# Optimization experiments

Measured on AMD Instinct MI355X. Metric: run time of the kernel, lower is better.

Reference implementation:

```python
import jax, jax.numpy as jnp
import numpy as np

B, TQ, TKV, D, H = 4, 512, 4096, 1024, 8
HEAD_DIM = D // H


def setup_inputs() -> dict:
    key = jax.random.key(0)
    ks = jax.random.split(key, 8)
    s = 0.02
    inputs_q = jax.random.normal(ks[0], (B, TQ, D), jnp.float32)
    inputs_kv = jax.random.normal(ks[1], (B, TKV, D), jnp.float32)
    attention_mask = jax.random.randint(ks[2], (B, TQ, TKV), 0, 2).astype(bool)
    Wq = jax.random.normal(ks[3], (D, D), jnp.float32) * s
    Wk = jax.random.normal(ks[4], (D, D), jnp.float32) * s
    Wv = jax.random.normal(ks[5], (D, D), jnp.float32) * s
    Wo = jax.random.normal(ks[6], (D, D), jnp.float32) * s
    zb = jnp.zeros((D,), jnp.float32)
    return {"inputs_q": inputs_q, "inputs_kv": inputs_kv, "attention_mask": attention_mask,
            "Wq": Wq, "bq": zb, "Wk": Wk, "bk": zb, "Wv": Wv, "bv": zb, "Wo": Wo, "bo": zb}


def _split_heads(x, h):
    b, t, c = x.shape
    return x.reshape(b, t, h, c // h).transpose(0, 2, 1, 3)  # b h t d


def reference(inputs_q, inputs_kv, attention_mask, Wq, bq, Wk, bk, Wv, bv, Wo, bo):
    q = _split_heads(inputs_q @ Wq + bq, H)   # [b,h,tq,d]
    k = _split_heads(inputs_kv @ Wk + bk, H)  # [b,h,tkv,d]
    v = _split_heads(inputs_kv @ Wv + bv, H)  # [b,h,tkv,d]
    scale = 1.0 / np.sqrt(HEAD_DIM).astype(np.float32)
    scores = jnp.einsum('bhtd,bhTd->bhtT', q, k) * scale
    large_k = jnp.asarray(1e30, scores.dtype)  # 1e30 for fp32 per source
    scores = jnp.where(attention_mask[:, None, :, :], scores, -large_k)
    probs = jax.nn.softmax(scores, axis=-1)
    summed = jnp.einsum('bhtT,bhTd->bhtd', probs, v)
    b, h, t, d = summed.shape
    summed = summed.transpose(0, 2, 1, 3).reshape(b, t, h * d)  # [b,tq,hiddens]
    # wipe rows whose mask is entirely zero (post-softmax wipe-masking)
    wipe = jnp.all(~attention_mask, axis=-1, keepdims=True)  # [b,tq,1]
    summed = jnp.where(wipe, jnp.zeros_like(summed), summed)
    return summed @ Wo + bo
```

## Files before the change

kernel.cpp:

```cpp
#include <hip/hip_runtime.h>
#include <cstdint>
#include <cstddef>

typedef unsigned short US;
typedef __bf16 bf16_t;
typedef bf16_t bf16x8 __attribute__((ext_vector_type(8)));
typedef float  f32x4  __attribute__((ext_vector_type(4)));
typedef US     us8    __attribute__((ext_vector_type(8)));
typedef US     us4    __attribute__((ext_vector_type(4)));

#define AS1 __attribute__((address_space(1)))
#define AS3 __attribute__((address_space(3)))

__device__ __forceinline__ void gl_lds16(const void* g, void* l) {
    __builtin_amdgcn_global_load_lds((AS1 unsigned int*)(size_t)g,
                                     (AS3 unsigned int*)l, 16, 0, 0);
}

__device__ __forceinline__ US f2bf(float f) {
    unsigned u = __builtin_bit_cast(unsigned, f);
    u += 0x7FFFu + ((u >> 16) & 1u);
    return (US)(u >> 16);
}

__device__ __forceinline__ float bf2f(US u) {
    return __builtin_bit_cast(float, (unsigned)u << 16);
}

__device__ __forceinline__ bf16x8 ldv8(const US* p) {
    return __builtin_bit_cast(bf16x8, *(const us8*)p);
}

__global__ void prep(const float* __restrict__ Xq, const float* __restrict__ Xkv,
                     const int* __restrict__ Mi, unsigned long long* __restrict__ MBits,
                     US* __restrict__ XqB, US* __restrict__ XkvB,
                     const float* __restrict__ Wq, const float* __restrict__ Wk,
                     const float* __restrict__ Wv, const float* __restrict__ Wo,
                     US* __restrict__ WTbase) {
    __shared__ float t[32][33];
    const int b = blockIdx.x, tid = threadIdx.x;

    for (int u = b; u < 18432; u += 4096) {
        if (u < 2048) {
            int i = u * 256 + tid;
            float4 f = ((const float4*)Xq)[i];
            us4 o = { f2bf(f.x), f2bf(f.y), f2bf(f.z), f2bf(f.w) };
            ((us4*)XqB)[i] = o;
        } else {
            int i = (u - 2048) * 256 + tid;
            float4 f = ((const float4*)Xkv)[i];
            us4 o = { f2bf(f.x), f2bf(f.y), f2bf(f.z), f2bf(f.w) };
            ((us4*)XkvB)[i] = o;
        }
    }

    for (int u = b; u < 32768; u += 4096) {
        int i = u * 256 + tid;
        int m = Mi[i];
        unsigned long long bits = __ballot(m != 0);
        if ((tid & 63) == 0) MBits[i >> 6] = bits;
    }

    {
        int z = b >> 10, rr = b & 1023;
        int bx = rr & 31, by = rr >> 5;
        const float* W = (z == 0) ? Wq : (z == 1) ? Wk : (z == 2) ? Wv : Wo;
        US* WT = WTbase + (size_t)z * 1024 * 1024;
        int tx = tid & 31, ty = tid >> 5;
        int x = bx * 32 + tx;
#pragma unroll
        for (int r = 0; r < 4; ++r)
            t[ty + r * 8][tx] = W[(size_t)(by * 32 + ty + r * 8) * 1024 + x];
        __syncthreads();
        int nx = by * 32 + tx;
#pragma unroll
        for (int r = 0; r < 4; ++r)
            WT[(size_t)(bx * 32 + ty + r * 8) * 1024 + nx] = f2bf(t[tx][ty + r * 8]);
    }
}

template <int MODE, int BM>
__global__ __launch_bounds__(256, 2)
void gemm_bt(const US* __restrict__ A, const US* __restrict__ Bt,
             const float* __restrict__ bias, void* __restrict__ out,
             int tlog2, float scale) {
    constexpr int K = 1024, N = 1024, BK = 64;
    constexpr int MI = BM / 32;
    __shared__ US As[BM * BK];
    __shared__ US Bs[128 * BK];
    const int tid = threadIdx.x;
    const int wv = tid >> 6, ln = tid & 63;
    const int g = ln >> 4, c15 = ln & 15;
    const int m0 = blockIdx.x * BM, n0 = blockIdx.y * 128;
    const int wm = (wv & 1) * (BM / 2), wn = (wv >> 1) * 64;

    f32x4 acc[MI][4];
    const f32x4 z = {0.f, 0.f, 0.f, 0.f};
#pragma unroll
    for (int i = 0; i < MI; ++i)
#pragma unroll
        for (int j = 0; j < 4; ++j) acc[i][j] = z;

    const US* Ab = A + (size_t)m0 * K;
    const US* Bb = Bt + (size_t)n0 * K;

    for (int k0 = 0; k0 < K; k0 += BK) {
        __syncthreads();
#pragma unroll
        for (int q = 0; q < BM / 32; ++q) {
            int eb = (q * 256 + wv * 64) * 8;
            int r = (eb >> 6) + (ln >> 3);
            int sw = (ln & 7) ^ (r & 7);
            gl_lds16(Ab + (size_t)r * K + k0 + sw * 8, &As[eb]);
        }
#pragma unroll
        for (int q = 0; q < 4; ++q) {
            int eb = (q * 256 + wv * 64) * 8;
            int r = (eb >> 6) + (ln >> 3);
            int sw = (ln & 7) ^ (r & 7);
            gl_lds16(Bb + (size_t)r * K + k0 + sw * 8, &Bs[eb]);
        }
        __syncthreads();
#pragma unroll
        for (int ks = 0; ks < 2; ++ks) {
            bf16x8 a[MI], b[4];
#pragma unroll
            for (int i = 0; i < MI; ++i) {
                int p = (ks * 4 + g) ^ (c15 & 7);
                a[i] = ldv8(&As[(wm + i * 16 + c15) * BK + p * 8]);
            }
#pragma unroll
            for (int j = 0; j < 4; ++j) {
                int p = (ks * 4 + g) ^ (c15 & 7);
                b[j] = ldv8(&Bs[(wn + j * 16 + c15) * BK + p * 8]);
            }
#pragma unroll
            for (int i = 0; i < MI; ++i)
#pragma unroll
                for (int j = 0; j < 4; ++j)
                    acc[i][j] = __builtin_amdgcn_mfma_f32_16x16x32_bf16(a[i], b[j], acc[i][j], 0, 0, 0);
        }
    }

#pragma unroll
    for (int i = 0; i < MI; ++i) {
#pragma unroll
        for (int j = 0; j < 4; ++j) {
            int col = n0 + wn + j * 16 + c15;
            float bvv = bias[col];
#pragma unroll
            for (int r = 0; r < 4; ++r) {
                int row = m0 + wm + i * 16 + g * 4 + r;
                float v = (acc[i][j][r] + bvv) * scale;
                if (MODE == 0) {
                    int b_ = row >> tlog2;
                    int t = row & ((1 << tlog2) - 1);
                    int h = col >> 7, d = col & 127;
                    ((US*)out)[(((size_t)(b_ * 8 + h) << tlog2) + t) * 128 + d] = f2bf(v);
                } else {
                    ((float*)out)[(size_t)row * N + col] = v;
                }
            }
        }
    }
}

__global__ __launch_bounds__(256, 2)
void gemm_kv(const US* __restrict__ A, const US* __restrict__ BtK,
             const US* __restrict__ BtV, const float* __restrict__ bk,
             const float* __restrict__ bv, US* __restrict__ Kout,
             US* __restrict__ VTout) {
    constexpr int K = 1024, BK = 64;
    __shared__ US lds[3 * 128 * BK];
    US* As  = lds;
    US* BsK = lds + 128 * BK;
    US* BsV = lds + 2 * 128 * BK;
    const int tid = threadIdx.x;
    const int wv = tid >> 6, ln = tid & 63;
    const int g = ln >> 4, c15 = ln & 15;
    const int m0 = blockIdx.x * 128, n0 = blockIdx.y * 128;
    const int wm = (wv & 1) * 64, wn = (wv >> 1) * 64;

    f32x4 aK[4][4], aV[4][4];
    const f32x4 z = {0.f, 0.f, 0.f, 0.f};
#pragma unroll
    for (int i = 0; i < 4; ++i)
#pragma unroll
        for (int j = 0; j < 4; ++j) { aK[i][j] = z; aV[i][j] = z; }

    const US* Ab  = A   + (size_t)m0 * K;
    const US* BbK = BtK + (size_t)n0 * K;
    const US* BbV = BtV + (size_t)n0 * K;

    for (int k0 = 0; k0 < K; k0 += BK) {
        __syncthreads();
#pragma unroll
        for (int q = 0; q < 4; ++q) {
            int eb = (q * 256 + wv * 64) * 8;
            int r = (eb >> 6) + (ln >> 3);
            int sw = (ln & 7) ^ (r & 7);
            gl_lds16(Ab  + (size_t)r * K + k0 + sw * 8, &As[eb]);
            gl_lds16(BbK + (size_t)r * K + k0 + sw * 8, &BsK[eb]);
            gl_lds16(BbV + (size_t)r * K + k0 + sw * 8, &BsV[eb]);
        }
        __syncthreads();
#pragma unroll
        for (int ks = 0; ks < 2; ++ks) {
            bf16x8 a[4], bK[4], bV[4];
#pragma unroll
            for (int i = 0; i < 4; ++i) {
                int p = (ks * 4 + g) ^ (c15 & 7);
                a[i] = ldv8(&As[(wm + i * 16 + c15) * BK + p * 8]);
            }
#pragma unroll
            for (int j = 0; j < 4; ++j) {
                int p = (ks * 4 + g) ^ (c15 & 7);
                bK[j] = ldv8(&BsK[(wn + j * 16 + c15) * BK + p * 8]);
                bV[j] = ldv8(&BsV[(wn + j * 16 + c15) * BK + p * 8]);
            }
#pragma unroll
            for (int i = 0; i < 4; ++i)
#pragma unroll
                for (int j = 0; j < 4; ++j) {
                    aK[i][j] = __builtin_amdgcn_mfma_f32_16x16x32_bf16(a[i], bK[j], aK[i][j], 0, 0, 0);
                    aV[i][j] = __builtin_amdgcn_mfma_f32_16x16x32_bf16(a[i], bV[j], aV[i][j], 0, 0, 0);
                }
        }
    }

    const int h = n0 >> 7;
    const int b_ = m0 >> 12, tbase = m0 & 4095;

#pragma unroll
    for (int i = 0; i < 4; ++i) {
#pragma unroll
        for (int j = 0; j < 4; ++j) {
            int col = n0 + wn + j * 16 + c15;
            float bkv = bk[col];
            int d = col & 127;
#pragma unroll
            for (int r = 0; r < 4; ++r) {
                int row = m0 + wm + i * 16 + g * 4 + r;
                int t = row & 4095;
                Kout[(((size_t)(b_ * 8 + h) << 12) + t) * 128 + d] = f2bf(aK[i][j][r] + bkv);
            }
        }
    }

    __syncthreads();
    US* T = lds;
#pragma unroll
    for (int i = 0; i < 4; ++i) {
#pragma unroll
        for (int j = 0; j < 4; ++j) {
            int dcol = wn + j * 16 + c15;
            float bvv = bv[n0 + dcol];
#pragma unroll
            for (int r = 0; r < 4; ++r) {
                int kvrow = wm + i * 16 + g * 4 + r;
                T[dcol * 136 + kvrow] = f2bf(aV[i][j][r] + bvv);
            }
        }
    }
    __syncthreads();
    {
        int d = tid >> 1, half = (tid & 1) * 64;
        US* vrow = VTout + ((size_t)(b_ * 8 + h) * 128 + d) * 4096 + tbase + half;
        const US* tr = &T[d * 136 + half];
#pragma unroll
        for (int s = 0; s < 8; ++s)
            *(us8*)(vrow + s * 8) = *(const us8*)(tr + s * 8);
    }
}

__global__ __launch_bounds__(256, 3)
void flash(const US* __restrict__ Qh, const US* __restrict__ Kh,
           const US* __restrict__ VTh, const unsigned long long* __restrict__ MBits,
           US* __restrict__ Opart, float* __restrict__ Lpart) {
    __shared__ US Ks[64 * 128];
    __shared__ US Vs[128 * 64];
    __shared__ US Ps[4][32 * 64];
    const int tid = threadIdx.x, wv = tid >> 6, ln = tid & 63;
    const int g = ln >> 4, c15 = ln & 15;
    const int bid = blockIdx.x;
    const int qt = bid / 192;
    const int rest = bid - qt * 192;
    const int bh = rest / 6, sp = rest - bh * 6;
    const int qbase = qt * 128;
    const int b_ = bh >> 3;
    const int t0 = (sp < 4) ? sp * 11 : 44 + (sp - 4) * 10;
    const int nt = (sp < 4) ? 11 : 10;
    const int wq = wv * 32;

    bf16x8 qa[2][4];
#pragma unroll
    for (int ib = 0; ib < 2; ++ib) {
        const US* qrow = Qh + ((size_t)bh * 512 + qbase + wq + ib * 16 + c15) * 128;
#pragma unroll
        for (int ks = 0; ks < 4; ++ks)
            qa[ib][ks] = ldv8(qrow + ks * 32 + g * 8);
    }

    f32x4 o[8][2];
    const f32x4 z = {0.f, 0.f, 0.f, 0.f};
#pragma unroll
    for (int d = 0; d < 8; ++d) { o[d][0] = z; o[d][1] = z; }
    float l2[2] = {0.f, 0.f};

    const unsigned long long* Mrow[2];
    Mrow[0] = MBits + (size_t)(b_ * 512 + qbase + wq + c15) * 64;
    Mrow[1] = Mrow[0] + (size_t)16 * 64;
    const US* Kbase = Kh + ((size_t)bh * 4096 + (size_t)t0 * 64) * 128;
    const US* Vbase = VTh + (size_t)bh * 128 * 4096;
    US* Pw = &Ps[wv][0];

    for (int t = 0; t < nt; ++t) {
        int kv0 = (t0 + t) * 64;
        __syncthreads();
        const US* Kb = Kbase + (size_t)t * 64 * 128;
#pragma unroll
        for (int q = 0; q < 4; ++q) {
            int eb = (q * 256 + wv * 64) * 8;
            int r = (eb >> 7) + (ln >> 4);
            int sw = (ln & 15) ^ (r & 15);
            gl_lds16(Kb + (size_t)r * 128 + sw * 8, &Ks[eb]);
        }
#pragma unroll
        for (int q = 0; q < 4; ++q) {
            int eb = (q * 256 + wv * 64) * 8;
            int r = (eb >> 6) + (ln >> 3);
            int sw = (ln & 7) ^ (r & 7);
            gl_lds16(Vbase + (size_t)r * 4096 + kv0 + sw * 8, &Vs[eb]);
        }
        unsigned long long m64[2];
        m64[0] = Mrow[0][t0 + t];
        m64[1] = Mrow[1][t0 + t];
        __syncthreads();

#pragma unroll
        for (int kb = 0; kb < 4; ++kb) {
            f32x4 s0 = z, s1 = z;
#pragma unroll
            for (int ks = 0; ks < 4; ++ks) {
                bf16x8 kf = ldv8(&Ks[(kb * 16 + c15) * 128 + (((ks * 4 + g) ^ c15) * 8)]);
                s0 = __builtin_amdgcn_mfma_f32_16x16x32_bf16(kf, qa[0][ks], s0, 0, 0, 0);
                s1 = __builtin_amdgcn_mfma_f32_16x16x32_bf16(kf, qa[1][ks], s1, 0, 0, 0);
            }
            int cw = kb * 4 + g;
#pragma unroll
            for (int ib = 0; ib < 2; ++ib) {
                f32x4 sv = ib ? s1 : s0;
                unsigned mq = (unsigned)(m64[ib] >> (kb * 16 + g * 4)) & 15u;
                float p0 = (mq & 1u) ? __expf(sv[0]) : 0.f;
                float p1 = (mq & 2u) ? __expf(sv[1]) : 0.f;
                float p2 = (mq & 4u) ? __expf(sv[2]) : 0.f;
                float p3 = (mq & 8u) ? __expf(sv[3]) : 0.f;
                l2[ib] += (p0 + p1) + (p2 + p3);
                int q = ib * 16 + c15;
                US* wp = Pw + q * 64 + (((cw >> 1) ^ (q & 7)) * 8) + (cw & 1) * 4;
                us4 pv = { f2bf(p0), f2bf(p1), f2bf(p2), f2bf(p3) };
                *(us4*)wp = pv;
            }
        }

#pragma unroll
        for (int ks = 0; ks < 2; ++ks) {
            bf16x8 pf[2];
#pragma unroll
            for (int ib = 0; ib < 2; ++ib) {
                int q = ib * 16 + c15;
                pf[ib] = ldv8(&Pw[q * 64 + (((ks * 4 + g) ^ (q & 7)) * 8)]);
            }
#pragma unroll
            for (int d = 0; d < 8; ++d) {
                bf16x8 vf = ldv8(&Vs[(d * 16 + c15) * 64 + (((ks * 4 + g) ^ (c15 & 7)) * 8)]);
                o[d][0] = __builtin_amdgcn_mfma_f32_16x16x32_bf16(vf, pf[0], o[d][0], 0, 0, 0);
                o[d][1] = __builtin_amdgcn_mfma_f32_16x16x32_bf16(vf, pf[1], o[d][1], 0, 0, 0);
            }
        }
    }

    float lf[2];
#pragma unroll
    for (int ib = 0; ib < 2; ++ib) {
        float l = l2[ib];
        l += __shfl_xor(l, 16); l += __shfl_xor(l, 32);
        lf[ib] = l;
    }
    if (ln < 16) {
        size_t lb = ((size_t)sp * 32 + bh) * 512 + qbase + wq + c15;
        Lpart[lb] = lf[0];
        Lpart[lb + 16] = lf[1];
    }
    US* Ob = Opart + (((size_t)sp * 32 + bh) * 128 + g * 4) * 512 + qbase + wq + c15;
#pragma unroll
    for (int d = 0; d < 8; ++d)
#pragma unroll
        for (int r = 0; r < 4; ++r) {
            Ob[(size_t)(d * 16 + r) * 512] = f2bf(o[d][0][r]);
            Ob[(size_t)(d * 16 + r) * 512 + 16] = f2bf(o[d][1][r]);
        }
}

__global__ void combine(const US* __restrict__ Opart, const float* __restrict__ Lpart,
                        US* __restrict__ AO) {
    __shared__ float linv[128];
    __shared__ float T[128 * 33];
    const int qt = blockIdx.x, bh = blockIdx.y;
    const int b_ = bh >> 3, h = bh & 7;
    const int tid = threadIdx.x;
    const size_t spstride = (size_t)32 * 128 * 512;

    if (tid < 128) {
        float s = 0.f;
#pragma unroll
        for (int sp = 0; sp < 6; ++sp)
            s += Lpart[((size_t)sp * 32 + bh) * 512 + qt * 128 + tid];
        linv[tid] = (s > 0.f) ? 1.f / s : 0.f;
    }
    __syncthreads();

    for (int ds0 = 0; ds0 < 128; ds0 += 32) {
        if (ds0) __syncthreads();
        {
            int d = ds0 + (tid >> 3);
            int q0 = (tid & 7) * 16;
            const US* base = Opart + ((size_t)bh * 128 + d) * 512 + qt * 128 + q0;
            float acc[16];
#pragma unroll
            for (int i = 0; i < 16; ++i) acc[i] = 0.f;
#pragma unroll
            for (int sp = 0; sp < 6; ++sp) {
                us8 a = *(const us8*)(base + sp * spstride);
                us8 b = *(const us8*)(base + sp * spstride + 8);
#pragma unroll
                for (int i = 0; i < 8; ++i) {
                    acc[i] += bf2f(a[i]);
                    acc[8 + i] += bf2f(b[i]);
                }
            }
            int dd = d - ds0;
#pragma unroll
            for (int i = 0; i < 16; ++i)
                T[(q0 + i) * 33 + dd] = acc[i] * linv[q0 + i];
        }
        __syncthreads();
#pragma unroll
        for (int it = 0; it < 4; ++it) {
            int idx = tid + it * 256;
            int q = idx >> 3, c = idx & 7;
            const float* tr = &T[q * 33 + c * 4];
            us4 ov = { f2bf(tr[0]), f2bf(tr[1]), f2bf(tr[2]), f2bf(tr[3]) };
            *(us4*)(AO + ((size_t)(b_ * 512 + qt * 128 + q)) * 1024 + h * 128 + ds0 + c * 4) = ov;
        }
    }
}

extern "C" void kernel_launch(void* const* d_in, const int* in_sizes, int n_in,
                              void* d_out, int out_size, void* d_ws, size_t ws_size,
                              hipStream_t stream) {
    (void)in_sizes; (void)n_in; (void)out_size; (void)ws_size;
    const float* Xq  = (const float*)d_in[0];
    const float* Xkv = (const float*)d_in[1];
    const int*   Mi  = (const int*)d_in[2];
    const float* Wq  = (const float*)d_in[3];
    const float* bq  = (const float*)d_in[4];
    const float* Wk  = (const float*)d_in[5];
    const float* bk  = (const float*)d_in[6];
    const float* Wv  = (const float*)d_in[7];
    const float* bv  = (const float*)d_in[8];
    const float* Wo  = (const float*)d_in[9];
    const float* bo  = (const float*)d_in[10];
    float* out = (float*)d_out;

    char* p = (char*)d_ws;
    US* WT   = (US*)p; p += (size_t)4 * 1024 * 1024 * 2;
    US* AO   = (US*)p; p += (size_t)2048 * 1024 * 2;
    US* XqB  = (US*)p; p += (size_t)2048 * 1024 * 2;
    US* Qh   = (US*)p; p += (size_t)2048 * 1024 * 2;
    US* Kh   = (US*)p; p += (size_t)16384 * 1024 * 2;
    US* VTh  = (US*)p; p += (size_t)16384 * 1024 * 2;
    US* XkvB = (US*)p; p += (size_t)16384 * 1024 * 2;
    unsigned long long* MBits = (unsigned long long*)p; p += (size_t)131072 * 8;
    US* Opart    = XkvB;
    float* Lpart = (float*)XqB;

    prep<<<4096, 256, 0, stream>>>(Xq, Xkv, Mi, MBits, XqB, XkvB, Wq, Wk, Wv, Wo, WT);

    gemm_bt<0, 64><<<dim3(32, 8), 256, 0, stream>>>(XqB, WT, bq, Qh, 9, 0.08838834764831843f);
    gemm_kv<<<dim3(128, 8), 256, 0, stream>>>(XkvB, WT + 1048576, WT + 2097152,
                                              bk, bv, Kh, VTh);
    flash<<<768, 256, 0, stream>>>(Qh, Kh, VTh, MBits, Opart, Lpart);
    combine<<<dim3(4, 32), 256, 0, stream>>>(Opart, Lpart, AO);
    gemm_bt<1, 64><<<dim3(32, 8), 256, 0, stream>>>(AO, WT + 3145728, bo, out, 0, 1.0f);
}
```

Before: 340.5 us.

## Double flash query tile per block and split KV into eight chunks

Each flash block now processes 256 query rows, 64 per wave, instead of 128, so every K/V tile staged in LDS is reused across twice as many queries. The KV sequence is split into 8 equal chunks of 8 tiles, replacing the uneven 6-way split, and the grid shrinks from 768 to 512 blocks. The combine kernel now sums 8 partials. The cost is roughly double the accumulator and Q-fragment registers, a doubled P buffer in LDS, and occupancy lowered from 3 to 2 blocks per CU, which reduces latency hiding.

```diff
diff --git a/kernel.cpp b/kernel.cpp
--- a/kernel.cpp
+++ b/kernel.cpp
@@ -273,48 +273,50 @@
     }
 }
 
-__global__ __launch_bounds__(256, 3)
+__global__ __launch_bounds__(256, 2)
 void flash(const US* __restrict__ Qh, const US* __restrict__ Kh,
            const US* __restrict__ VTh, const unsigned long long* __restrict__ MBits,
            US* __restrict__ Opart, float* __restrict__ Lpart) {
     __shared__ US Ks[64 * 128];
     __shared__ US Vs[128 * 64];
-    __shared__ US Ps[4][32 * 64];
+    __shared__ US Ps[4][64 * 64];
     const int tid = threadIdx.x, wv = tid >> 6, ln = tid & 63;
     const int g = ln >> 4, c15 = ln & 15;
     const int bid = blockIdx.x;
-    const int qt = bid / 192;
-    const int rest = bid - qt * 192;
-    const int bh = rest / 6, sp = rest - bh * 6;
-    const int qbase = qt * 128;
+    const int qt = bid >> 8;
+    const int rest = bid & 255;
+    const int bh = rest >> 3, sp = rest & 7;
+    const int qbase = qt * 256;
     const int b_ = bh >> 3;
-    const int t0 = (sp < 4) ? sp * 11 : 44 + (sp - 4) * 10;
-    const int nt = (sp < 4) ? 11 : 10;
-    const int wq = wv * 32;
-
-    bf16x8 qa[2][4];
-#pragma unroll
-    for (int ib = 0; ib < 2; ++ib) {
+    const int t0 = sp * 8;
+    const int wq = wv * 64;
+
+    bf16x8 qa[4][4];
+#pragma unroll
+    for (int ib = 0; ib < 4; ++ib) {
         const US* qrow = Qh + ((size_t)bh * 512 + qbase + wq + ib * 16 + c15) * 128;
 #pragma unroll
         for (int ks = 0; ks < 4; ++ks)
             qa[ib][ks] = ldv8(qrow + ks * 32 + g * 8);
     }
 
-    f32x4 o[8][2];
+    f32x4 o[8][4];
     const f32x4 z = {0.f, 0.f, 0.f, 0.f};
 #pragma unroll
-    for (int d = 0; d < 8; ++d) { o[d][0] = z; o[d][1] = z; }
-    float l2[2] = {0.f, 0.f};
-
-    const unsigned long long* Mrow[2];
+    for (int d = 0; d < 8; ++d)
+#pragma unroll
+        for (int ib = 0; ib < 4; ++ib) o[d][ib] = z;
+    float l4[4] = {0.f, 0.f, 0.f, 0.f};
+
+    const unsigned long long* Mrow[4];
     Mrow[0] = MBits + (size_t)(b_ * 512 + qbase + wq + c15) * 64;
-    Mrow[1] = Mrow[0] + (size_t)16 * 64;
+#pragma unroll
+    for (int ib = 1; ib < 4; ++ib) Mrow[ib] = Mrow[0] + (size_t)ib * 16 * 64;
     const US* Kbase = Kh + ((size_t)bh * 4096 + (size_t)t0 * 64) * 128;
     const US* Vbase = VTh + (size_t)bh * 128 * 4096;
     US* Pw = &Ps[wv][0];
 
-    for (int t = 0; t < nt; ++t) {
+    for (int t = 0; t < 8; ++t) {
         int kv0 = (t0 + t) * 64;
         __syncthreads();
         const US* Kb = Kbase + (size_t)t * 64 * 128;
@@ -332,30 +334,32 @@
             int sw = (ln & 7) ^ (r & 7);
             gl_lds16(Vbase + (size_t)r * 4096 + kv0 + sw * 8, &Vs[eb]);
         }
-        unsigned long long m64[2];
-        m64[0] = Mrow[0][t0 + t];
-        m64[1] = Mrow[1][t0 + t];
+        unsigned long long m64[4];
+#pragma unroll
+        for (int ib = 0; ib < 4; ++ib) m64[ib] = Mrow[ib][t0 + t];
         __syncthreads();
 
 #pragma unroll
         for (int kb = 0; kb < 4; ++kb) {
-            f32x4 s0 = z, s1 = z;
+            f32x4 s[4];
+#pragma unroll
+            for (int ib = 0; ib < 4; ++ib) s[ib] = z;
 #pragma unroll
             for (int ks = 0; ks < 4; ++ks) {
                 bf16x8 kf = ldv8(&Ks[(kb * 16 + c15) * 128 + (((ks * 4 + g) ^ c15) * 8)]);
-                s0 = __builtin_amdgcn_mfma_f32_16x16x32_bf16(kf, qa[0][ks], s0, 0, 0, 0);
-                s1 = __builtin_amdgcn_mfma_f32_16x16x32_bf16(kf, qa[1][ks], s1, 0, 0, 0);
+#pragma unroll
+                for (int ib = 0; ib < 4; ++ib)
+                    s[ib] = __builtin_amdgcn_mfma_f32_16x16x32_bf16(kf, qa[ib][ks], s[ib], 0, 0, 0);
             }
             int cw = kb * 4 + g;
 #pragma unroll
-            for (int ib = 0; ib < 2; ++ib) {
-                f32x4 sv = ib ? s1 : s0;
+            for (int ib = 0; ib < 4; ++ib) {
                 unsigned mq = (unsigned)(m64[ib] >> (kb * 16 + g * 4)) & 15u;
-                float p0 = (mq & 1u) ? __expf(sv[0]) : 0.f;
-                float p1 = (mq & 2u) ? __expf(sv[1]) : 0.f;
-                float p2 = (mq & 4u) ? __expf(sv[2]) : 0.f;
-                float p3 = (mq & 8u) ? __expf(sv[3]) : 0.f;
-                l2[ib] += (p0 + p1) + (p2 + p3);
+                float p0 = (mq & 1u) ? __expf(s[ib][0]) : 0.f;
+                float p1 = (mq & 2u) ? __expf(s[ib][1]) : 0.f;
+                float p2 = (mq & 4u) ? __expf(s[ib][2]) : 0.f;
+                float p3 = (mq & 8u) ? __expf(s[ib][3]) : 0.f;
+                l4[ib] += (p0 + p1) + (p2 + p3);
                 int q = ib * 16 + c15;
                 US* wp = Pw + q * 64 + (((cw >> 1) ^ (q & 7)) * 8) + (cw & 1) * 4;
                 us4 pv = { f2bf(p0), f2bf(p1), f2bf(p2), f2bf(p3) };
@@ -365,41 +369,42 @@
 
 #pragma unroll
         for (int ks = 0; ks < 2; ++ks) {
-            bf16x8 pf[2];
-#pragma unroll
-            for (int ib = 0; ib < 2; ++ib) {
+            bf16x8 pf[4];
+#pragma unroll
+            for (int ib = 0; ib < 4; ++ib) {
                 int q = ib * 16 + c15;
                 pf[ib] = ldv8(&Pw[q * 64 + (((ks * 4 + g) ^ (q & 7)) * 8)]);
             }
 #pragma unroll
             for (int d = 0; d < 8; ++d) {
                 bf16x8 vf = ldv8(&Vs[(d * 16 + c15) * 64 + (((ks * 4 + g) ^ (c15 & 7)) * 8)]);
-                o[d][0] = __builtin_amdgcn_mfma_f32_16x16x32_bf16(vf, pf[0], o[d][0], 0, 0, 0);
-                o[d][1] = __builtin_amdgcn_mfma_f32_16x16x32_bf16(vf, pf[1], o[d][1], 0, 0, 0);
-            }
-        }
-    }
-
-    float lf[2];
-#pragma unroll
-    for (int ib = 0; ib < 2; ++ib) {
-        float l = l2[ib];
+#pragma unroll
+                for (int ib = 0; ib < 4; ++ib)
+                    o[d][ib] = __builtin_amdgcn_mfma_f32_16x16x32_bf16(vf, pf[ib], o[d][ib], 0, 0, 0);
+            }
+        }
+    }
+
+    float lf[4];
+#pragma unroll
+    for (int ib = 0; ib < 4; ++ib) {
+        float l = l4[ib];
         l += __shfl_xor(l, 16); l += __shfl_xor(l, 32);
         lf[ib] = l;
     }
     if (ln < 16) {
         size_t lb = ((size_t)sp * 32 + bh) * 512 + qbase + wq + c15;
-        Lpart[lb] = lf[0];
-        Lpart[lb + 16] = lf[1];
+#pragma unroll
+        for (int ib = 0; ib < 4; ++ib) Lpart[lb + ib * 16] = lf[ib];
     }
     US* Ob = Opart + (((size_t)sp * 32 + bh) * 128 + g * 4) * 512 + qbase + wq + c15;
 #pragma unroll
     for (int d = 0; d < 8; ++d)
 #pragma unroll
-        for (int r = 0; r < 4; ++r) {
-            Ob[(size_t)(d * 16 + r) * 512] = f2bf(o[d][0][r]);
-            Ob[(size_t)(d * 16 + r) * 512 + 16] = f2bf(o[d][1][r]);
-        }
+        for (int r = 0; r < 4; ++r)
+#pragma unroll
+            for (int ib = 0; ib < 4; ++ib)
+                Ob[(size_t)(d * 16 + r) * 512 + ib * 16] = f2bf(o[d][ib][r]);
 }
 
 __global__ void combine(const US* __restrict__ Opart, const float* __restrict__ Lpart,
@@ -414,7 +419,7 @@
     if (tid < 128) {
         float s = 0.f;
 #pragma unroll
-        for (int sp = 0; sp < 6; ++sp)
+        for (int sp = 0; sp < 8; ++sp)
             s += Lpart[((size_t)sp * 32 + bh) * 512 + qt * 128 + tid];
         linv[tid] = (s > 0.f) ? 1.f / s : 0.f;
     }
@@ -430,7 +435,7 @@
 #pragma unroll
             for (int i = 0; i < 16; ++i) acc[i] = 0.f;
 #pragma unroll
-            for (int sp = 0; sp < 6; ++sp) {
+            for (int sp = 0; sp < 8; ++sp) {
                 us8 a = *(const us8*)(base + sp * spstride);
                 us8 b = *(const us8*)(base + sp * spstride + 8);
 #pragma unroll
@@ -490,7 +495,7 @@
     gemm_bt<0, 64><<<dim3(32, 8), 256, 0, stream>>>(XqB, WT, bq, Qh, 9, 0.08838834764831843f);
     gemm_kv<<<dim3(128, 8), 256, 0, stream>>>(XkvB, WT + 1048576, WT + 2097152,
                                               bk, bv, Kh, VTh);
-    flash<<<768, 256, 0, stream>>>(Qh, Kh, VTh, MBits, Opart, Lpart);
+    flash<<<512, 256, 0, stream>>>(Qh, Kh, VTh, MBits, Opart, Lpart);
     combine<<<dim3(4, 32), 256, 0, stream>>>(Opart, Lpart, AO);
     gemm_bt<1, 64><<<dim3(32, 8), 256, 0, stream>>>(AO, WT + 3145728, bo, out, 0, 1.0f);
 }
```

Result: slower. 436.3 us (+28.2%).

## Transpose mask bits and partial outputs for coalesced attention writes and combine

Applied to the files above, without the earlier changes.

Stores the packed mask bits as [batch][kv-tile][query] so each wave's per-tile mask loads come from contiguous addresses. The attention kernel now stages its bf16 output through the swizzled P scratch in shared memory and writes query-major partial outputs with 16-byte stores, replacing scattered 2-byte stores. The combine kernel then reads the partials row-contiguously and drops its shared-memory transpose and extra barriers. This reuses the Ps buffer after the main loop, which adds some LDS traffic at the end of the attention kernel.

```diff
diff --git a/kernel.cpp b/kernel.cpp
--- a/kernel.cpp
+++ b/kernel.cpp
@@ -58,7 +58,10 @@
         int i = u * 256 + tid;
         int m = Mi[i];
         unsigned long long bits = __ballot(m != 0);
-        if ((tid & 63) == 0) MBits[i >> 6] = bits;
+        if ((tid & 63) == 0) {
+            int b_ = i >> 21, q = (i >> 12) & 511, kt = (i & 4095) >> 6;
+            MBits[((size_t)(b_ * 64 + kt)) * 512 + q] = bits;
+        }
     }
 
     {
@@ -307,9 +310,7 @@
     for (int d = 0; d < 8; ++d) { o[d][0] = z; o[d][1] = z; }
     float l2[2] = {0.f, 0.f};
 
-    const unsigned long long* Mrow[2];
-    Mrow[0] = MBits + (size_t)(b_ * 512 + qbase + wq + c15) * 64;
-    Mrow[1] = Mrow[0] + (size_t)16 * 64;
+    const unsigned long long* Mb = MBits + (size_t)(b_ * 64) * 512 + qbase + wq + c15;
     const US* Kbase = Kh + ((size_t)bh * 4096 + (size_t)t0 * 64) * 128;
     const US* Vbase = VTh + (size_t)bh * 128 * 4096;
     US* Pw = &Ps[wv][0];
@@ -333,8 +334,8 @@
             gl_lds16(Vbase + (size_t)r * 4096 + kv0 + sw * 8, &Vs[eb]);
         }
         unsigned long long m64[2];
-        m64[0] = Mrow[0][t0 + t];
-        m64[1] = Mrow[1][t0 + t];
+        m64[0] = Mb[(size_t)(t0 + t) * 512];
+        m64[1] = Mb[(size_t)(t0 + t) * 512 + 16];
         __syncthreads();
 
 #pragma unroll
@@ -392,67 +393,69 @@
         Lpart[lb] = lf[0];
         Lpart[lb + 16] = lf[1];
     }
-    US* Ob = Opart + (((size_t)sp * 32 + bh) * 128 + g * 4) * 512 + qbase + wq + c15;
-#pragma unroll
-    for (int d = 0; d < 8; ++d)
-#pragma unroll
-        for (int r = 0; r < 4; ++r) {
-            Ob[(size_t)(d * 16 + r) * 512] = f2bf(o[d][0][r]);
-            Ob[(size_t)(d * 16 + r) * 512 + 16] = f2bf(o[d][1][r]);
-        }
+
+    size_t obase = (((size_t)sp * 32 + bh) * 512 + qbase + wq) * 128;
+#pragma unroll
+    for (int half = 0; half < 2; ++half) {
+#pragma unroll
+        for (int d = 0; d < 4; ++d) {
+            int dg = half * 4 + d;
+            int c = d * 2 + (g >> 1), sub = g & 1;
+#pragma unroll
+            for (int ib = 0; ib < 2; ++ib) {
+                int q = ib * 16 + c15;
+                us4 pv = { f2bf(o[dg][ib][0]), f2bf(o[dg][ib][1]),
+                           f2bf(o[dg][ib][2]), f2bf(o[dg][ib][3]) };
+                *(us4*)&Pw[q * 64 + ((c ^ (q & 7)) * 8) + sub * 4] = pv;
+            }
+        }
+#pragma unroll
+        for (int p = 0; p < 4; ++p) {
+            int q = p * 8 + (ln >> 3);
+            int oct = ln & 7;
+            us8 v = *(const us8*)&Pw[q * 64 + ((oct ^ (q & 7)) * 8)];
+            *(us8*)(Opart + obase + (size_t)q * 128 + half * 64 + oct * 8) = v;
+        }
+    }
 }
 
 __global__ void combine(const US* __restrict__ Opart, const float* __restrict__ Lpart,
                         US* __restrict__ AO) {
     __shared__ float linv[128];
-    __shared__ float T[128 * 33];
     const int qt = blockIdx.x, bh = blockIdx.y;
     const int b_ = bh >> 3, h = bh & 7;
     const int tid = threadIdx.x;
-    const size_t spstride = (size_t)32 * 128 * 512;
+    const size_t spO = (size_t)32 * 512 * 128;
+    const size_t spL = (size_t)32 * 512;
 
     if (tid < 128) {
         float s = 0.f;
 #pragma unroll
         for (int sp = 0; sp < 6; ++sp)
-            s += Lpart[((size_t)sp * 32 + bh) * 512 + qt * 128 + tid];
+            s += Lpart[sp * spL + (size_t)bh * 512 + qt * 128 + tid];
         linv[tid] = (s > 0.f) ? 1.f / s : 0.f;
     }
     __syncthreads();
 
-    for (int ds0 = 0; ds0 < 128; ds0 += 32) {
-        if (ds0) __syncthreads();
-        {
-            int d = ds0 + (tid >> 3);
-            int q0 = (tid & 7) * 16;
-            const US* base = Opart + ((size_t)bh * 128 + d) * 512 + qt * 128 + q0;
-            float acc[16];
-#pragma unroll
-            for (int i = 0; i < 16; ++i) acc[i] = 0.f;
-#pragma unroll
-            for (int sp = 0; sp < 6; ++sp) {
-                us8 a = *(const us8*)(base + sp * spstride);
-                us8 b = *(const us8*)(base + sp * spstride + 8);
-#pragma unroll
-                for (int i = 0; i < 8; ++i) {
-                    acc[i] += bf2f(a[i]);
-                    acc[8 + i] += bf2f(b[i]);
-                }
-            }
-            int dd = d - ds0;
-#pragma unroll
-            for (int i = 0; i < 16; ++i)
-                T[(q0 + i) * 33 + dd] = acc[i] * linv[q0 + i];
-        }
-        __syncthreads();
-#pragma unroll
-        for (int it = 0; it < 4; ++it) {
-            int idx = tid + it * 256;
-            int q = idx >> 3, c = idx & 7;
-            const float* tr = &T[q * 33 + c * 4];
-            us4 ov = { f2bf(tr[0]), f2bf(tr[1]), f2bf(tr[2]), f2bf(tr[3]) };
-            *(us4*)(AO + ((size_t)(b_ * 512 + qt * 128 + q)) * 1024 + h * 128 + ds0 + c * 4) = ov;
-        }
+#pragma unroll
+    for (int p = 0; p < 8; ++p) {
+        int ql = p * 16 + (tid >> 4);
+        int d = (tid & 15) * 8;
+        const US* base = Opart + ((size_t)bh * 512 + qt * 128 + ql) * 128 + d;
+        float acc[8];
+#pragma unroll
+        for (int i = 0; i < 8; ++i) acc[i] = 0.f;
+#pragma unroll
+        for (int sp = 0; sp < 6; ++sp) {
+            us8 v = *(const us8*)(base + sp * spO);
+#pragma unroll
+            for (int i = 0; i < 8; ++i) acc[i] += bf2f(v[i]);
+        }
+        float iv = linv[ql];
+        us8 ov;
+#pragma unroll
+        for (int i = 0; i < 8; ++i) ov[i] = f2bf(acc[i] * iv);
+        *(us8*)(AO + ((size_t)(b_ * 512 + qt * 128 + ql)) * 1024 + h * 128 + d) = ov;
     }
 }
 
```

New measurement: 354.1 us. 1.04x slower.
